# Kernel tuning notes

Measured on AMD Instinct MI355X. Metric: run time of the kernel, lower is better.

## Reference

```python
import jax, jax.numpy as jnp
import numpy as np

INF = jnp.float32(1e9)


def _nearest_zero_dist_axis0(is_zero):
    """1D distance (in index units) to the nearest True along axis 0.

    is_zero: bool array [L, ...]. Returns float32 [L, ...].
    """
    d0 = jnp.where(is_zero, jnp.float32(0.0), INF)

    def step(c, d):
        c = jnp.minimum(c + 1.0, d)
        return c, c

    init = jnp.full(d0.shape[1:], INF, dtype=jnp.float32)
    _, fwd = jax.lax.scan(step, init, d0)
    _, bwd = jax.lax.scan(step, init, d0[::-1])
    return jnp.minimum(fwd, bwd[::-1])


def _minplus_parabola_axis0(g2):
    """Exact squared-EDT lower envelope along axis 0.

    g2: float32 [L, ...] of squared distances. Returns
    out[i, ...] = min_k ( (i-k)^2 + g2[k, ...] ).
    Brute-force min-plus, scanned over output index to bound memory.
    """
    L = g2.shape[0]
    k = jnp.arange(L, dtype=jnp.float32)

    def step(_, i):
        # (i - k)^2 broadcast against all source positions k
        par = (i - k) ** 2  # [L]
        par = par.reshape((L,) + (1,) * (g2.ndim - 1))
        return None, jnp.min(par + g2, axis=0)  # [...]

    _, out = jax.lax.scan(step, None, jnp.arange(L, dtype=jnp.float32))
    return out  # [L, ...]


def _edt(x):
    """Exact N-D Euclidean distance transform matching scipy's
    distance_transform_edt: distance from each nonzero element to the
    nearest zero element, over all dims of x."""
    is_zero = (x == 0)
    # Pass 1 (axis 0): exact 1D distance to nearest zero along axis 0.
    d = _nearest_zero_dist_axis0(is_zero)  # [B,H,W]
    d2 = d * d
    # Passes 2..n: exact min-plus with squared parabola along each
    # remaining axis, applied to the running squared distance field.
    for ax in range(1, x.ndim):
        d2 = jnp.moveaxis(d2, ax, 0)
        d2 = _minplus_parabola_axis0(d2)
        d2 = jnp.moveaxis(d2, 0, ax)
    return jnp.sqrt(d2)


def setup_inputs() -> dict:
    key = jax.random.key(0)
    B, H, W = 16, 512, 512
    x = (jax.random.uniform(key, (B, H, W)) > 0.05).astype(jnp.float32)
    return {"x": x}


def reference(x) -> jnp.ndarray:
    distance = _edt(x)
    # distance[x.isnan()] = nan  (NaN inputs are nonzero -> foreground,
    # then their output is masked to NaN, as in the torch module)
    return jnp.where(jnp.isnan(x), jnp.nan, distance)
```

## Files before the change

### kernel.cpp

```cpp
#include <hip/hip_runtime.h>
#include <math.h>
#include <stdint.h>

#define NB 16
#define NH 512
#define NW 512
#define PLANE (NH * NW)
#define INF_D 1.0e9f
#define INF2 1.0e18f
#define BIG 3.0e38f
#define NSEG 64
#define TWB 8
#define HROW 516

__device__ __forceinline__ void eval_seg(const float* __restrict__ hrow,
                                         int ss, float* best,
                                         const float* neg2i) {
    const float* hp = hrow + ss * 8;
    float4 A = *reinterpret_cast<const float4*>(hp);
    float4 B = *reinterpret_cast<const float4*>(hp + 4);
    float s8f = (float)(ss * 8);
#pragma unroll
    for (int j = 0; j < 8; ++j) {
        float n2 = neg2i[j];
        float c0 = fmaf(n2, s8f, A.x);
        float c1 = fmaf(n2, s8f + 1.0f, A.y);
        float c2 = fmaf(n2, s8f + 2.0f, A.z);
        float c3 = fmaf(n2, s8f + 3.0f, A.w);
        float c4 = fmaf(n2, s8f + 4.0f, B.x);
        float c5 = fmaf(n2, s8f + 5.0f, B.y);
        float c6 = fmaf(n2, s8f + 6.0f, B.z);
        float c7 = fmaf(n2, s8f + 7.0f, B.w);
        float bb = fminf(fminf(best[j], c0), c1);
        bb = fminf(fminf(bb, c2), c3);
        bb = fminf(fminf(bb, c4), c5);
        bb = fminf(fminf(bb, c6), c7);
        best[j] = bb;
    }
}

__device__ __forceinline__ void eval_minplus(const float* __restrict__ hrow,
                                             int q, float* best,
                                             const float* neg2i,
                                             const float* ifl) {
    int s_lo0 = (q > 0) ? q - 1 : 0;
    int s_hi0 = (q < NSEG - 1) ? q + 1 : NSEG - 1;
    for (int ss = s_lo0; ss <= s_hi0; ++ss) eval_seg(hrow, ss, best, neg2i);

    float t0 = fmaf(ifl[0], ifl[0], best[0]);
    float t1 = fmaf(ifl[1], ifl[1], best[1]);
    float t2 = fmaf(ifl[2], ifl[2], best[2]);
    float t3 = fmaf(ifl[3], ifl[3], best[3]);
    float t4 = fmaf(ifl[4], ifl[4], best[4]);
    float t5 = fmaf(ifl[5], ifl[5], best[5]);
    float t6 = fmaf(ifl[6], ifl[6], best[6]);
    float t7 = fmaf(ifl[7], ifl[7], best[7]);
    float m = fmaxf(fmaxf(t0, t1), t2);
    m = fmaxf(fmaxf(m, t3), t4);
    m = fmaxf(fmaxf(m, t5), t6);
    float bmax = fmaxf(m, t7);

    int sw = (int)sqrtf(bmax) + 1;
    int i0 = q * 8;
    int s_lo = (i0 - sw) >> 3;
    int s_hi = (i0 + 7 + sw) >> 3;
    if (s_lo < 0) s_lo = 0;
    if (s_hi > NSEG - 1) s_hi = NSEG - 1;
    for (int ss = s_lo; ss <= s_hi; ++ss) {
        if (ss >= s_lo0 && ss <= s_hi0) continue;
        eval_seg(hrow, ss, best, neg2i);
    }
}

__global__ __launch_bounds__(256, 4) void k_pass_b(const float* __restrict__ x,
                                                   unsigned char* __restrict__ code) {
    int col = blockIdx.x * 256 + threadIdx.x;
    float d0[NB], dd[NB];
    int nanb = 0;
#pragma unroll
    for (int b = 0; b < NB; ++b) {
        float v = x[(size_t)b * PLANE + col];
        nanb |= (isnan(v) ? (1 << b) : 0);
        d0[b] = (v == 0.0f) ? 0.0f : INF_D;
    }
    float cc = INF_D;
#pragma unroll
    for (int b = 0; b < NB; ++b) { cc = fminf(cc + 1.0f, d0[b]); dd[b] = cc; }
    cc = INF_D;
#pragma unroll
    for (int b = NB - 1; b >= 0; --b) { cc = fminf(cc + 1.0f, d0[b]); dd[b] = fminf(dd[b], cc); }
#pragma unroll
    for (int b = 0; b < NB; ++b) {
        int di = (dd[b] >= 1.0e8f) ? 31 : (int)dd[b];
        code[(size_t)b * PLANE + col] =
            (unsigned char)(di | (((nanb >> b) & 1) << 7));
    }
}

__global__ __launch_bounds__(512, 4) void k_pass_h(const unsigned char* __restrict__ code,
                                                   float* __restrict__ out) {
    __shared__ float hs[TWB * HROW];
    __shared__ unsigned int flgw[NH * 2];
    int t = threadIdx.x;
    int b = blockIdx.y;
    int w0 = blockIdx.x * TWB;
    const unsigned char* gb8 = code + (size_t)b * PLANE + w0;

    for (int m = t; m < 1024; m += 512) {
        int k = m >> 1;
        int bo = (m & 1) * 4;
        unsigned int u = *reinterpret_cast<const unsigned int*>(gb8 + (size_t)k * NW + bo);
        int kk = k * k;
#pragma unroll
        for (int e = 0; e < 4; ++e) {
            int c = (u >> (8 * e)) & 0xFF;
            int dl = c & 31;
            hs[(bo + e) * HROW + k] = (dl == 31) ? INF2 : (float)(dl * dl + kk);
        }
        flgw[m] = (u >> 7) & 0x01010101u;
    }
    __syncthreads();

    int w = t & 7, q = t >> 3;
    int i0 = q * 8;
    float best[8], neg2i[8], ifl[8];
#pragma unroll
    for (int j = 0; j < 8; ++j) {
        best[j] = BIG;
        ifl[j] = (float)(i0 + j);
        neg2i[j] = (float)(-2 * (i0 + j));
    }
    eval_minplus(&hs[w * HROW], q, best, neg2i, ifl);

    const unsigned char* flgb = reinterpret_cast<const unsigned char*>(flgw);
    float wgf = (float)(w0 + w);
    float* ob = out + (size_t)b * PLANE + w0 + w;
#pragma unroll
    for (int j = 0; j < 8; ++j) {
        float v = fmaf(ifl[j], ifl[j], best[j]);
        float v2 = fmaf(wgf, wgf, v);
        unsigned int bits = __float_as_uint(v2) |
                            ((unsigned int)flgb[(i0 + j) * TWB + w] << 31);
        ob[(size_t)(i0 + j) * NW] = __uint_as_float(bits);
    }
}

__global__ __launch_bounds__(512, 4) void k_pass_w(float* __restrict__ out) {
    __shared__ float hs[TWB * HROW];
    __shared__ unsigned int flgw[NH * 2];
    int t = threadIdx.x;
    int line0 = blockIdx.x * TWB;
    float* gb = out + (size_t)line0 * NW;

    for (int m = t; m < 1024; m += 512) {
        float4 v = *reinterpret_cast<const float4*>(gb + (size_t)m * 4);
        int line = m >> 7;
        int k = (m * 4) & 511;
        unsigned int u0 = __float_as_uint(v.x), u1 = __float_as_uint(v.y);
        unsigned int u2 = __float_as_uint(v.z), u3 = __float_as_uint(v.w);
        flgw[m] = (u0 >> 31) | ((u1 >> 31) << 8) |
                  ((u2 >> 31) << 16) | ((u3 >> 31) << 24);
        float4 o;
        o.x = __uint_as_float(u0 & 0x7fffffffu);
        o.y = __uint_as_float(u1 & 0x7fffffffu);
        o.z = __uint_as_float(u2 & 0x7fffffffu);
        o.w = __uint_as_float(u3 & 0x7fffffffu);
        *reinterpret_cast<float4*>(&hs[line * HROW + k]) = o;
    }
    __syncthreads();

    int line = t & 7, q = t >> 3;
    int i0 = q * 8;
    float best[8], neg2i[8], ifl[8];
#pragma unroll
    for (int j = 0; j < 8; ++j) {
        best[j] = BIG;
        ifl[j] = (float)(i0 + j);
        neg2i[j] = (float)(-2 * (i0 + j));
    }
    eval_minplus(&hs[line * HROW], q, best, neg2i, ifl);

    unsigned int f0 = flgw[(line * NW + i0) >> 2];
    unsigned int f1 = flgw[((line * NW + i0) >> 2) + 1];
    float v[8];
#pragma unroll
    for (int j = 0; j < 8; ++j) {
        float m = fmaf(ifl[j], ifl[j], best[j]);
        float sq = sqrtf(m);
        unsigned int fb = (j < 4) ? ((f0 >> (8 * j)) & 1u)
                                  : ((f1 >> (8 * (j - 4))) & 1u);
        v[j] = fb ? __builtin_nanf("") : sq;
    }
    float* op = gb + (size_t)line * NW + i0;
    float4 oa, ob4;
    oa.x = v[0]; oa.y = v[1]; oa.z = v[2]; oa.w = v[3];
    ob4.x = v[4]; ob4.y = v[5]; ob4.z = v[6]; ob4.w = v[7];
    *reinterpret_cast<float4*>(op) = oa;
    *reinterpret_cast<float4*>(op + 4) = ob4;
}

extern "C" void kernel_launch(void* const* d_in, const int* in_sizes, int n_in,
                              void* d_out, int out_size, void* d_ws, size_t ws_size,
                              hipStream_t stream) {
    (void)in_sizes; (void)n_in; (void)out_size; (void)ws_size;
    const float* x = (const float*)d_in[0];
    float* out = (float*)d_out;
    unsigned char* code = (unsigned char*)d_ws;

    k_pass_b<<<dim3(PLANE / 256), 256, 0, stream>>>(x, code);
    k_pass_h<<<dim3(NW / TWB, NB), 512, 0, stream>>>(code, out);
    k_pass_w<<<dim3(NB * NH / TWB), 512, 0, stream>>>(out);
}
```

Baseline: 36.51 us.

## Reorder EDT passes: H first, fuse W and batch passes, ring-search pruning

Drops the separate batch-axis pass. The H pass now reads x directly and computes the min-plus from zero positions, using a ring search that expands outward with per-segment minimum pruning. The W pass and the batch-axis min-plus over 16 planes are fused in one kernel per row h, which loads all 16 batch lines into shared memory. This cuts one launch and one global round trip, but it lowers the block count for the fused kernel (512 blocks) and adds a larger shared footprint and data-dependent ring loops.

After: 52.90 us. 44.9% more time.

```diff
diff --git a/kernel.cpp b/kernel.cpp
--- a/kernel.cpp
+++ b/kernel.cpp
@@ -6,7 +6,6 @@
 #define NH 512
 #define NW 512
 #define PLANE (NH * NW)
-#define INF_D 1.0e9f
 #define INF2 1.0e18f
 #define BIG 3.0e38f
 #define NSEG 64
@@ -39,14 +38,7 @@
     }
 }
 
-__device__ __forceinline__ void eval_minplus(const float* __restrict__ hrow,
-                                             int q, float* best,
-                                             const float* neg2i,
-                                             const float* ifl) {
-    int s_lo0 = (q > 0) ? q - 1 : 0;
-    int s_hi0 = (q < NSEG - 1) ? q + 1 : NSEG - 1;
-    for (int ss = s_lo0; ss <= s_hi0; ++ss) eval_seg(hrow, ss, best, neg2i);
-
+__device__ __forceinline__ float bmax8(const float* best, const float* ifl) {
     float t0 = fmaf(ifl[0], ifl[0], best[0]);
     float t1 = fmaf(ifl[1], ifl[1], best[1]);
     float t2 = fmaf(ifl[2], ifl[2], best[2]);
@@ -58,8 +50,36 @@
     float m = fmaxf(fmaxf(t0, t1), t2);
     m = fmaxf(fmaxf(m, t3), t4);
     m = fmaxf(fmaxf(m, t5), t6);
-    float bmax = fmaxf(m, t7);
-
+    return fmaxf(m, t7);
+}
+
+__device__ __forceinline__ void eval_ring(const float* __restrict__ hrow,
+                                          const float* __restrict__ sminw,
+                                          int q, float* best,
+                                          const float* neg2i,
+                                          const float* ifl) {
+    float bmax = BIG;
+    for (int step = 0; step < 2 * NSEG - 1; ++step) {
+        int r = (step + 1) >> 1;
+        float gapf = (float)(8 * (r - 1) + 1);
+        float gap2 = gapf * gapf;
+        if ((step & 1) && gap2 >= bmax) break;
+        int s = (step & 1) ? (q - r) : (q + r);
+        if (s < 0 || s >= NSEG) continue;
+        if (step && (gap2 + sminw[s * TWB] >= bmax)) continue;
+        eval_seg(hrow, s, best, neg2i);
+        bmax = bmax8(best, ifl);
+    }
+}
+
+__device__ __forceinline__ void eval_window(const float* __restrict__ hrow,
+                                            int q, float* best,
+                                            const float* neg2i,
+                                            const float* ifl) {
+    int s_lo0 = (q > 0) ? q - 1 : 0;
+    int s_hi0 = (q < NSEG - 1) ? q + 1 : NSEG - 1;
+    for (int ss = s_lo0; ss <= s_hi0; ++ss) eval_seg(hrow, ss, best, neg2i);
+    float bmax = bmax8(best, ifl);
     int sw = (int)sqrtf(bmax) + 1;
     int i0 = q * 8;
     int s_lo = (i0 - sw) >> 3;
@@ -72,52 +92,44 @@
     }
 }
 
-__global__ __launch_bounds__(256, 4) void k_pass_b(const float* __restrict__ x,
-                                                   unsigned char* __restrict__ code) {
-    int col = blockIdx.x * 256 + threadIdx.x;
-    float d0[NB], dd[NB];
-    int nanb = 0;
-#pragma unroll
-    for (int b = 0; b < NB; ++b) {
-        float v = x[(size_t)b * PLANE + col];
-        nanb |= (isnan(v) ? (1 << b) : 0);
-        d0[b] = (v == 0.0f) ? 0.0f : INF_D;
-    }
-    float cc = INF_D;
-#pragma unroll
-    for (int b = 0; b < NB; ++b) { cc = fminf(cc + 1.0f, d0[b]); dd[b] = cc; }
-    cc = INF_D;
-#pragma unroll
-    for (int b = NB - 1; b >= 0; --b) { cc = fminf(cc + 1.0f, d0[b]); dd[b] = fminf(dd[b], cc); }
-#pragma unroll
-    for (int b = 0; b < NB; ++b) {
-        int di = (dd[b] >= 1.0e8f) ? 31 : (int)dd[b];
-        code[(size_t)b * PLANE + col] =
-            (unsigned char)(di | (((nanb >> b) & 1) << 7));
-    }
-}
-
-__global__ __launch_bounds__(512, 4) void k_pass_h(const unsigned char* __restrict__ code,
-                                                   float* __restrict__ out) {
+__global__ __launch_bounds__(512, 4) void k_pass_h(const float* __restrict__ x,
+                                                   float* __restrict__ ws) {
     __shared__ float hs[TWB * HROW];
+    __shared__ float smin[NSEG * TWB];
     __shared__ unsigned int flgw[NH * 2];
     int t = threadIdx.x;
     int b = blockIdx.y;
     int w0 = blockIdx.x * TWB;
-    const unsigned char* gb8 = code + (size_t)b * PLANE + w0;
+    const float* xb = x + (size_t)b * PLANE + w0;
 
     for (int m = t; m < 1024; m += 512) {
         int k = m >> 1;
-        int bo = (m & 1) * 4;
-        unsigned int u = *reinterpret_cast<const unsigned int*>(gb8 + (size_t)k * NW + bo);
-        int kk = k * k;
+        int half = m & 1;
+        float4 v = *reinterpret_cast<const float4*>(xb + (size_t)k * NW + half * 4);
+        float kk = (float)(k * k);
+        unsigned int f = 0;
 #pragma unroll
         for (int e = 0; e < 4; ++e) {
-            int c = (u >> (8 * e)) & 0xFF;
-            int dl = c & 31;
-            hs[(bo + e) * HROW + k] = (dl == 31) ? INF2 : (float)(dl * dl + kk);
-        }
-        flgw[m] = (u >> 7) & 0x01010101u;
+            float val = (&v.x)[e];
+            int w = half * 4 + e;
+            hs[w * HROW + k] = (val == 0.0f) ? kk : INF2;
+            f |= (isnan(val) ? 1u : 0u) << (8 * e);
+        }
+        flgw[m] = f;
+    }
+    __syncthreads();
+    {
+        int s = t >> 3, w = t & 7;
+        const float* hp = &hs[w * HROW + s * 8];
+        float4 A = *reinterpret_cast<const float4*>(hp);
+        float4 B = *reinterpret_cast<const float4*>(hp + 4);
+        int k0 = s * 8;
+        float m0 = fminf(fminf(A.x - (float)(k0 * k0), A.y - (float)((k0 + 1) * (k0 + 1))),
+                         A.z - (float)((k0 + 2) * (k0 + 2)));
+        float m1 = fminf(fminf(A.w - (float)((k0 + 3) * (k0 + 3)), B.x - (float)((k0 + 4) * (k0 + 4))),
+                         B.y - (float)((k0 + 5) * (k0 + 5)));
+        float m2 = fminf(B.z - (float)((k0 + 6) * (k0 + 6)), B.w - (float)((k0 + 7) * (k0 + 7)));
+        smin[t] = fminf(fminf(m0, m1), m2);
     }
     __syncthreads();
 
@@ -130,11 +142,11 @@
         ifl[j] = (float)(i0 + j);
         neg2i[j] = (float)(-2 * (i0 + j));
     }
-    eval_minplus(&hs[w * HROW], q, best, neg2i, ifl);
+    eval_ring(&hs[w * HROW], &smin[w], q, best, neg2i, ifl);
 
     const unsigned char* flgb = reinterpret_cast<const unsigned char*>(flgw);
     float wgf = (float)(w0 + w);
-    float* ob = out + (size_t)b * PLANE + w0 + w;
+    float* ob = ws + (size_t)b * PLANE + w0 + w;
 #pragma unroll
     for (int j = 0; j < 8; ++j) {
         float v = fmaf(ifl[j], ifl[j], best[j]);
@@ -145,17 +157,18 @@
     }
 }
 
-__global__ __launch_bounds__(512, 4) void k_pass_w(float* __restrict__ out) {
-    __shared__ float hs[TWB * HROW];
-    __shared__ unsigned int flgw[NH * 2];
+__global__ __launch_bounds__(512, 4) void k_pass_wb(const float* __restrict__ ws,
+                                                    float* __restrict__ out) {
+    __shared__ float hs[NB * HROW];
+    __shared__ unsigned int flgw[NB * NW / 4];
     int t = threadIdx.x;
-    int line0 = blockIdx.x * TWB;
-    float* gb = out + (size_t)line0 * NW;
-
-    for (int m = t; m < 1024; m += 512) {
-        float4 v = *reinterpret_cast<const float4*>(gb + (size_t)m * 4);
+    int h = blockIdx.x;
+
+    for (int m = t; m < 2048; m += 512) {
         int line = m >> 7;
-        int k = (m * 4) & 511;
+        int k4 = (m & 127) * 4;
+        float4 v = *reinterpret_cast<const float4*>(
+            ws + (size_t)line * PLANE + (size_t)h * NW + k4);
         unsigned int u0 = __float_as_uint(v.x), u1 = __float_as_uint(v.y);
         unsigned int u2 = __float_as_uint(v.z), u3 = __float_as_uint(v.w);
         flgw[m] = (u0 >> 31) | ((u1 >> 31) << 8) |
@@ -165,38 +178,64 @@
         o.y = __uint_as_float(u1 & 0x7fffffffu);
         o.z = __uint_as_float(u2 & 0x7fffffffu);
         o.w = __uint_as_float(u3 & 0x7fffffffu);
-        *reinterpret_cast<float4*>(&hs[line * HROW + k]) = o;
-    }
-    __syncthreads();
-
-    int line = t & 7, q = t >> 3;
-    int i0 = q * 8;
-    float best[8], neg2i[8], ifl[8];
-#pragma unroll
-    for (int j = 0; j < 8; ++j) {
-        best[j] = BIG;
-        ifl[j] = (float)(i0 + j);
-        neg2i[j] = (float)(-2 * (i0 + j));
-    }
-    eval_minplus(&hs[line * HROW], q, best, neg2i, ifl);
-
-    unsigned int f0 = flgw[(line * NW + i0) >> 2];
-    unsigned int f1 = flgw[((line * NW + i0) >> 2) + 1];
-    float v[8];
-#pragma unroll
-    for (int j = 0; j < 8; ++j) {
-        float m = fmaf(ifl[j], ifl[j], best[j]);
-        float sq = sqrtf(m);
-        unsigned int fb = (j < 4) ? ((f0 >> (8 * j)) & 1u)
-                                  : ((f1 >> (8 * (j - 4))) & 1u);
-        v[j] = fb ? __builtin_nanf("") : sq;
-    }
-    float* op = gb + (size_t)line * NW + i0;
-    float4 oa, ob4;
-    oa.x = v[0]; oa.y = v[1]; oa.z = v[2]; oa.w = v[3];
-    ob4.x = v[4]; ob4.y = v[5]; ob4.z = v[6]; ob4.w = v[7];
-    *reinterpret_cast<float4*>(op) = oa;
-    *reinterpret_cast<float4*>(op + 4) = ob4;
+        *reinterpret_cast<float4*>(&hs[line * HROW + k4]) = o;
+    }
+    __syncthreads();
+
+    int lineA = t >> 6;
+    int qA = t & 63;
+    int lineB = lineA + 8;
+    int qB = qA;
+    float resA[8], resB[8];
+    {
+        int i0 = qA * 8;
+        float best[8], neg2i[8], ifl[8];
+#pragma unroll
+        for (int j = 0; j < 8; ++j) {
+            best[j] = BIG;
+            ifl[j] = (float)(i0 + j);
+            neg2i[j] = (float)(-2 * (i0 + j));
+        }
+        eval_window(&hs[lineA * HROW], qA, best, neg2i, ifl);
+#pragma unroll
+        for (int j = 0; j < 8; ++j) resA[j] = fmaf(ifl[j], ifl[j], best[j]);
+    }
+    {
+        int i0 = qB * 8;
+        float best[8], neg2i[8], ifl[8];
+#pragma unroll
+        for (int j = 0; j < 8; ++j) {
+            best[j] = BIG;
+            ifl[j] = (float)(i0 + j);
+            neg2i[j] = (float)(-2 * (i0 + j));
+        }
+        eval_window(&hs[lineB * HROW], qB, best, neg2i, ifl);
+#pragma unroll
+        for (int j = 0; j < 8; ++j) resB[j] = fmaf(ifl[j], ifl[j], best[j]);
+    }
+    __syncthreads();
+#pragma unroll
+    for (int j = 0; j < 8; ++j) hs[lineA * HROW + qA * 8 + j] = resA[j];
+#pragma unroll
+    for (int j = 0; j < 8; ++j) hs[lineB * HROW + qB * 8 + j] = resB[j];
+    __syncthreads();
+
+    const unsigned char* flgb = reinterpret_cast<const unsigned char*>(flgw);
+    float d2c[NB];
+#pragma unroll
+    for (int b = 0; b < NB; ++b) d2c[b] = hs[b * HROW + t];
+#pragma unroll
+    for (int bp = 0; bp < NB; ++bp) {
+        float mm = BIG;
+#pragma unroll
+        for (int b = 0; b < NB; ++b) {
+            float db = (float)((bp - b) * (bp - b));
+            mm = fminf(mm, db + d2c[b]);
+        }
+        float sq = sqrtf(mm);
+        float o = flgb[bp * NW + t] ? __builtin_nanf("") : sq;
+        out[(size_t)bp * PLANE + (size_t)h * NW + t] = o;
+    }
 }
 
 extern "C" void kernel_launch(void* const* d_in, const int* in_sizes, int n_in,
@@ -205,9 +244,8 @@
     (void)in_sizes; (void)n_in; (void)out_size; (void)ws_size;
     const float* x = (const float*)d_in[0];
     float* out = (float*)d_out;
-    unsigned char* code = (unsigned char*)d_ws;
-
-    k_pass_b<<<dim3(PLANE / 256), 256, 0, stream>>>(x, code);
-    k_pass_h<<<dim3(NW / TWB, NB), 512, 0, stream>>>(code, out);
-    k_pass_w<<<dim3(NB * NH / TWB), 512, 0, stream>>>(out);
-}
+    float* ws = (float*)d_ws;
+
+    k_pass_h<<<dim3(NW / TWB, NB), 512, 0, stream>>>(x, ws);
+    k_pass_wb<<<dim3(NH), 512, 0, stream>>>(ws, out);
+}
```

## Reorder EDT passes into two kernels: H-scan first, then fused W and B

Applied to the files above, without the earlier changes.

The pass order changes. The first kernel now computes the exact 1D nearest-zero distance along H from the raw input, using per-segment masks and prefix/suffix reductions in shared memory, and stores a 16-bit code. A second kernel takes one H row across all 16 batches, runs the W min-plus parabola pass, then does a brute-force min-plus over the batch axis (16 elements) in registers before writing sqrt or NaN. This cuts three launches and a full float round trip to two launches with a smaller intermediate. In exchange it uses 1024-thread blocks with about 41 KB of shared memory and a quadratic batch pass. Because the squared EDT is separable, changing the pass order keeps the result exact.

Result: slower. 38.64 us (+5.8%).

```diff
diff --git a/kernel.cpp b/kernel.cpp
--- a/kernel.cpp
+++ b/kernel.cpp
@@ -6,11 +6,9 @@
 #define NH 512
 #define NW 512
 #define PLANE (NH * NW)
-#define INF_D 1.0e9f
 #define INF2 1.0e18f
 #define BIG 3.0e38f
 #define NSEG 64
-#define TWB 8
 #define HROW 516
 
 __device__ __forceinline__ void eval_seg(const float* __restrict__ hrow,
@@ -39,14 +37,13 @@
     }
 }
 
-__device__ __forceinline__ void eval_minplus(const float* __restrict__ hrow,
-                                             int q, float* best,
-                                             const float* neg2i,
-                                             const float* ifl) {
+__device__ __forceinline__ void eval_window(const float* __restrict__ hrow,
+                                            int q, float* best,
+                                            const float* neg2i,
+                                            const float* ifl) {
     int s_lo0 = (q > 0) ? q - 1 : 0;
     int s_hi0 = (q < NSEG - 1) ? q + 1 : NSEG - 1;
     for (int ss = s_lo0; ss <= s_hi0; ++ss) eval_seg(hrow, ss, best, neg2i);
-
     float t0 = fmaf(ifl[0], ifl[0], best[0]);
     float t1 = fmaf(ifl[1], ifl[1], best[1]);
     float t2 = fmaf(ifl[2], ifl[2], best[2]);
@@ -59,7 +56,6 @@
     m = fmaxf(fmaxf(m, t3), t4);
     m = fmaxf(fmaxf(m, t5), t6);
     float bmax = fmaxf(m, t7);
-
     int sw = (int)sqrtf(bmax) + 1;
     int i0 = q * 8;
     int s_lo = (i0 - sw) >> 3;
@@ -72,131 +68,125 @@
     }
 }
 
-__global__ __launch_bounds__(256, 4) void k_pass_b(const float* __restrict__ x,
-                                                   unsigned char* __restrict__ code) {
-    int col = blockIdx.x * 256 + threadIdx.x;
-    float d0[NB], dd[NB];
-    int nanb = 0;
-#pragma unroll
-    for (int b = 0; b < NB; ++b) {
-        float v = x[(size_t)b * PLANE + col];
-        nanb |= (isnan(v) ? (1 << b) : 0);
-        d0[b] = (v == 0.0f) ? 0.0f : INF_D;
-    }
-    float cc = INF_D;
-#pragma unroll
-    for (int b = 0; b < NB; ++b) { cc = fminf(cc + 1.0f, d0[b]); dd[b] = cc; }
-    cc = INF_D;
-#pragma unroll
-    for (int b = NB - 1; b >= 0; --b) { cc = fminf(cc + 1.0f, d0[b]); dd[b] = fminf(dd[b], cc); }
-#pragma unroll
-    for (int b = 0; b < NB; ++b) {
-        int di = (dd[b] >= 1.0e8f) ? 31 : (int)dd[b];
-        code[(size_t)b * PLANE + col] =
-            (unsigned char)(di | (((nanb >> b) & 1) << 7));
-    }
-}
-
-__global__ __launch_bounds__(512, 4) void k_pass_h(const unsigned char* __restrict__ code,
-                                                   float* __restrict__ out) {
-    __shared__ float hs[TWB * HROW];
-    __shared__ unsigned int flgw[NH * 2];
+__global__ __launch_bounds__(512, 4) void k_scan_h(const float* __restrict__ x,
+                                                   unsigned short* __restrict__ code) {
+    __shared__ float hs[8 * HROW];
+    __shared__ unsigned int flgw[1024];
+    __shared__ int lza[512], rza[512];
     int t = threadIdx.x;
     int b = blockIdx.y;
-    int w0 = blockIdx.x * TWB;
-    const unsigned char* gb8 = code + (size_t)b * PLANE + w0;
+    int w0 = blockIdx.x * 8;
+    const float* xb = x + (size_t)b * PLANE + w0;
 
     for (int m = t; m < 1024; m += 512) {
-        int k = m >> 1;
-        int bo = (m & 1) * 4;
-        unsigned int u = *reinterpret_cast<const unsigned int*>(gb8 + (size_t)k * NW + bo);
-        int kk = k * k;
+        int k = m >> 1, half = m & 1;
+        float4 v = *reinterpret_cast<const float4*>(xb + (size_t)k * NW + half * 4);
+        unsigned int f = 0;
 #pragma unroll
         for (int e = 0; e < 4; ++e) {
-            int c = (u >> (8 * e)) & 0xFF;
-            int dl = c & 31;
-            hs[(bo + e) * HROW + k] = (dl == 31) ? INF2 : (float)(dl * dl + kk);
+            float val = (&v.x)[e];
+            hs[(half * 4 + e) * HROW + k] = (val == 0.0f) ? 1.0f : 0.0f;
+            f |= (isnan(val) ? 1u : 0u) << (8 * e);
         }
-        flgw[m] = (u >> 7) & 0x01010101u;
+        flgw[m] = f;
     }
     __syncthreads();
 
     int w = t & 7, q = t >> 3;
+    int base = w * HROW + q * 8;
+    float4 A = *reinterpret_cast<const float4*>(&hs[base]);
+    float4 Bv = *reinterpret_cast<const float4*>(&hs[base + 4]);
+    unsigned int mask = 0;
+#pragma unroll
+    for (int e = 0; e < 4; ++e) mask |= ((&A.x)[e] == 1.0f ? 1u : 0u) << e;
+#pragma unroll
+    for (int e = 0; e < 4; ++e) mask |= ((&Bv.x)[e] == 1.0f ? 1u : 0u) << (e + 4);
+    lza[q * 8 + w] = mask ? (q * 8 + __ffs(mask) - 1) : (1 << 20);
+    rza[q * 8 + w] = mask ? (q * 8 + 31 - __clz(mask)) : -(1 << 20);
+
+    int fwd[8], bwd[8];
+    int run = 1 << 20;
+#pragma unroll
+    for (int e = 0; e < 8; ++e) { run = ((mask >> e) & 1) ? 0 : run + 1; fwd[e] = run; }
+    run = 1 << 20;
+#pragma unroll
+    for (int e = 7; e >= 0; --e) { run = ((mask >> e) & 1) ? 0 : run + 1; bwd[e] = run; }
+    __syncthreads();
+
+    int pmax = -(1 << 20);
+    for (int c = 0; c < q; ++c) pmax = max(pmax, rza[c * 8 + w]);
+    int smin = 1 << 20;
+    for (int c = q + 1; c < 64; ++c) smin = min(smin, lza[c * 8 + w]);
+
+    const unsigned char* flgb = reinterpret_cast<const unsigned char*>(flgw);
+#pragma unroll
+    for (int e = 0; e < 8; ++e) {
+        int i = q * 8 + e;
+        int d = min(min(fwd[e], bwd[e]), min(i - pmax, smin - i));
+        if (d > 511) d = 1023;
+        unsigned short o = (unsigned short)(d | ((flgb[i * 8 + w] & 1) << 15));
+        code[(size_t)b * PLANE + (size_t)i * NW + w0 + w] = o;
+    }
+}
+
+__global__ __launch_bounds__(1024, 2) void k_wb(const unsigned short* __restrict__ code,
+                                                float* __restrict__ out) {
+    __shared__ float hs[NB * HROW];
+    __shared__ unsigned char flg[NB * NW];
+    int t = threadIdx.x;
+    int h = blockIdx.x;
+
+    const unsigned int* cp = reinterpret_cast<const unsigned int*>(code);
+    for (int m = t; m < NB * NW / 2; m += 1024) {
+        int b = m >> 8;
+        int wp = m & 255;
+        unsigned int v = cp[((size_t)b * PLANE + (size_t)h * NW) / 2 + wp];
+        int wa = wp * 2;
+        int dl0 = v & 1023, dl1 = (v >> 16) & 1023;
+        unsigned short fpair = (unsigned short)(((v >> 15) & 1u) | (((v >> 31) & 1u) << 8));
+        *reinterpret_cast<unsigned short*>(&flg[b * NW + wa]) = fpair;
+        hs[b * HROW + wa] = (dl0 == 1023) ? INF2 : (float)(dl0 * dl0 + wa * wa);
+        hs[b * HROW + wa + 1] = (dl1 == 1023) ? INF2 : (float)(dl1 * dl1 + (wa + 1) * (wa + 1));
+    }
+    __syncthreads();
+
+    int line = t >> 6, q = t & 63;
     int i0 = q * 8;
-    float best[8], neg2i[8], ifl[8];
+    float res[8];
+    {
+        float best[8], neg2i[8], ifl[8];
+#pragma unroll
+        for (int j = 0; j < 8; ++j) {
+            best[j] = BIG;
+            ifl[j] = (float)(i0 + j);
+            neg2i[j] = (float)(-2 * (i0 + j));
+        }
+        eval_window(&hs[line * HROW], q, best, neg2i, ifl);
+#pragma unroll
+        for (int j = 0; j < 8; ++j) res[j] = fmaf(ifl[j], ifl[j], best[j]);
+    }
+    __syncthreads();
+#pragma unroll
+    for (int j = 0; j < 8; ++j) hs[line * HROW + i0 + j] = res[j];
+    __syncthreads();
+
+    int w = t & 511, g = t >> 9;
+    float d2c[NB];
+#pragma unroll
+    for (int b2 = 0; b2 < NB; ++b2) d2c[b2] = hs[b2 * HROW + w];
 #pragma unroll
     for (int j = 0; j < 8; ++j) {
-        best[j] = BIG;
-        ifl[j] = (float)(i0 + j);
-        neg2i[j] = (float)(-2 * (i0 + j));
-    }
-    eval_minplus(&hs[w * HROW], q, best, neg2i, ifl);
-
-    const unsigned char* flgb = reinterpret_cast<const unsigned char*>(flgw);
-    float wgf = (float)(w0 + w);
-    float* ob = out + (size_t)b * PLANE + w0 + w;
-#pragma unroll
-    for (int j = 0; j < 8; ++j) {
-        float v = fmaf(ifl[j], ifl[j], best[j]);
-        float v2 = fmaf(wgf, wgf, v);
-        unsigned int bits = __float_as_uint(v2) |
-                            ((unsigned int)flgb[(i0 + j) * TWB + w] << 31);
-        ob[(size_t)(i0 + j) * NW] = __uint_as_float(bits);
-    }
-}
-
-__global__ __launch_bounds__(512, 4) void k_pass_w(float* __restrict__ out) {
-    __shared__ float hs[TWB * HROW];
-    __shared__ unsigned int flgw[NH * 2];
-    int t = threadIdx.x;
-    int line0 = blockIdx.x * TWB;
-    float* gb = out + (size_t)line0 * NW;
-
-    for (int m = t; m < 1024; m += 512) {
-        float4 v = *reinterpret_cast<const float4*>(gb + (size_t)m * 4);
-        int line = m >> 7;
-        int k = (m * 4) & 511;
-        unsigned int u0 = __float_as_uint(v.x), u1 = __float_as_uint(v.y);
-        unsigned int u2 = __float_as_uint(v.z), u3 = __float_as_uint(v.w);
-        flgw[m] = (u0 >> 31) | ((u1 >> 31) << 8) |
-                  ((u2 >> 31) << 16) | ((u3 >> 31) << 24);
-        float4 o;
-        o.x = __uint_as_float(u0 & 0x7fffffffu);
-        o.y = __uint_as_float(u1 & 0x7fffffffu);
-        o.z = __uint_as_float(u2 & 0x7fffffffu);
-        o.w = __uint_as_float(u3 & 0x7fffffffu);
-        *reinterpret_cast<float4*>(&hs[line * HROW + k]) = o;
-    }
-    __syncthreads();
-
-    int line = t & 7, q = t >> 3;
-    int i0 = q * 8;
-    float best[8], neg2i[8], ifl[8];
-#pragma unroll
-    for (int j = 0; j < 8; ++j) {
-        best[j] = BIG;
-        ifl[j] = (float)(i0 + j);
-        neg2i[j] = (float)(-2 * (i0 + j));
-    }
-    eval_minplus(&hs[line * HROW], q, best, neg2i, ifl);
-
-    unsigned int f0 = flgw[(line * NW + i0) >> 2];
-    unsigned int f1 = flgw[((line * NW + i0) >> 2) + 1];
-    float v[8];
-#pragma unroll
-    for (int j = 0; j < 8; ++j) {
-        float m = fmaf(ifl[j], ifl[j], best[j]);
-        float sq = sqrtf(m);
-        unsigned int fb = (j < 4) ? ((f0 >> (8 * j)) & 1u)
-                                  : ((f1 >> (8 * (j - 4))) & 1u);
-        v[j] = fb ? __builtin_nanf("") : sq;
-    }
-    float* op = gb + (size_t)line * NW + i0;
-    float4 oa, ob4;
-    oa.x = v[0]; oa.y = v[1]; oa.z = v[2]; oa.w = v[3];
-    ob4.x = v[4]; ob4.y = v[5]; ob4.z = v[6]; ob4.w = v[7];
-    *reinterpret_cast<float4*>(op) = oa;
-    *reinterpret_cast<float4*>(op + 4) = ob4;
+        int bp = g * 8 + j;
+        float mm = BIG;
+#pragma unroll
+        for (int b2 = 0; b2 < NB; ++b2) {
+            float db = (float)((bp - b2) * (bp - b2));
+            mm = fminf(mm, db + d2c[b2]);
+        }
+        float sq = sqrtf(mm);
+        float o = flg[bp * NW + w] ? __builtin_nanf("") : sq;
+        out[(size_t)bp * PLANE + (size_t)h * NW + w] = o;
+    }
 }
 
 extern "C" void kernel_launch(void* const* d_in, const int* in_sizes, int n_in,
@@ -205,9 +195,8 @@
     (void)in_sizes; (void)n_in; (void)out_size; (void)ws_size;
     const float* x = (const float*)d_in[0];
     float* out = (float*)d_out;
-    unsigned char* code = (unsigned char*)d_ws;
-
-    k_pass_b<<<dim3(PLANE / 256), 256, 0, stream>>>(x, code);
-    k_pass_h<<<dim3(NW / TWB, NB), 512, 0, stream>>>(code, out);
-    k_pass_w<<<dim3(NB * NH / TWB), 512, 0, stream>>>(out);
-}
+    unsigned short* code = (unsigned short*)d_ws;
+
+    k_scan_h<<<dim3(NW / 8, NB), 512, 0, stream>>>(x, code);
+    k_wb<<<dim3(NH), 1024, 0, stream>>>(code, out);
+}
```
